# Optimization experiments

Hardware: AMD Instinct MI355X
Metric: run time of the kernel (lower is better)

The kernel has to match this reference:

```python
import jax, jax.numpy as jnp
import numpy as np

B, F, V, D_EMB = 16384, 32, 50000, 16
D_IN = F * D_EMB            # 512, concat embedding dim
N_TASK, N_SPEC, N_SH = 2, 2, 2
E = N_TASK * N_SPEC + N_SH  # 6 experts per CGC level
H1, H2 = 512, 256           # expert_params dims
T1, T2 = 128, 64            # tower dims


def setup_inputs() -> dict:
    key = jax.random.key(0)
    ks = iter(jax.random.split(key, 32))
    def w(shape, s=0.05):
        return jax.random.normal(next(ks), shape, jnp.float32) * s
    return dict(
        x_ids=jax.random.randint(next(ks), (B, F), 0, V),
        emb=w((F, V, D_EMB)),
        e1_W1=w((E, D_IN, H1)), e1_b1=jnp.zeros((E, H1), jnp.float32),
        e1_W2=w((E, H1, H2)), e1_b2=jnp.zeros((E, H2), jnp.float32),
        g1_Ws=w((N_TASK, D_IN, N_SPEC + N_SH)), g1_bs=jnp.zeros((N_TASK, N_SPEC + N_SH), jnp.float32),
        g1_Wsh=w((D_IN, E)), g1_bsh=jnp.zeros((E,), jnp.float32),
        e2_W1=w((E, H2, H1)), e2_b1=jnp.zeros((E, H1), jnp.float32),
        e2_W2=w((E, H1, H2)), e2_b2=jnp.zeros((E, H2), jnp.float32),
        g2_Ws=w((N_TASK, H2, N_SPEC + N_SH)), g2_bs=jnp.zeros((N_TASK, N_SPEC + N_SH), jnp.float32),
        tw_W1=w((N_TASK, H2, T1)), tw_b1=jnp.zeros((N_TASK, T1), jnp.float32),
        tw_W2=w((N_TASK, T1, T2)), tw_b2=jnp.zeros((N_TASK, T2), jnp.float32),
    )


def _cgc(x_list, W1, b1, W2, b2, Wg, bg, Wg_sh=None, bg_sh=None):
    # Stack expert inputs: task-t specific experts read x_list[t], shared read x_list[-1].
    X = jnp.stack([x_list[0]] * N_SPEC + [x_list[1]] * N_SPEC + [x_list[-1]] * N_SH)  # [E,B,Din]
    # Grouped two-layer expert MLP (BatchNorm is identity at eval-mode init).
    h = jax.nn.relu(jnp.einsum('ebd,edh->ebh', X, W1) + b1[:, None, :])   # [E,B,H1]
    out = jax.nn.relu(jnp.einsum('ebh,eho->ebo', h, W2) + b2[:, None, :])  # [E,B,H2]
    outs = []
    for t in range(N_TASK):
        gate = jax.nn.softmax(x_list[t] @ Wg[t] + bg[t], axis=-1)          # [B, N_SPEC+N_SH]
        sel = jnp.concatenate([out[t * N_SPEC:(t + 1) * N_SPEC], out[-N_SH:]], axis=0)
        outs.append(jnp.einsum('bk,kbo->bo', gate, sel))
    if Wg_sh is not None:  # shared gate only for levels < n_level
        gate = jax.nn.softmax(x_list[-1] @ Wg_sh + bg_sh, axis=-1)          # [B,E]
        outs.append(jnp.einsum('bk,kbo->bo', gate, out))
    return outs


def reference(x_ids, emb, e1_W1, e1_b1, e1_W2, e1_b2, g1_Ws, g1_bs, g1_Wsh, g1_bsh,
              e2_W1, e2_b1, e2_W2, e2_b2, g2_Ws, g2_bs, tw_W1, tw_b1, tw_W2, tw_b2):
    # Embedding lookup per sparse feature, then flatten (squeeze_dim=True).
    embed_x = emb[jnp.arange(F)[None, :], x_ids].reshape(B, D_IN)  # [B, 512]
    xs = [embed_x] * (N_TASK + 1)
    xs = _cgc(xs, e1_W1, e1_b1, e1_W2, e1_b2, g1_Ws, g1_bs, g1_Wsh, g1_bsh)  # level 1 -> 3 outs
    xs = _cgc(xs, e2_W1, e2_b1, e2_W2, e2_b2, g2_Ws, g2_bs)                  # level 2 -> 2 outs
    ys = []
    for t in range(N_TASK):
        h = jax.nn.relu(xs[t] @ tw_W1[t] + tw_b1[t])
        h = jax.nn.relu(h @ tw_W2[t] + tw_b2[t])
        ys.append(jax.nn.sigmoid(h))  # PredictionLayer('classification')
    return jnp.concatenate(ys, axis=1)  # [B, N_TASK*T2]
```

## Files before the change

### kernel.cpp

```cpp
#include <hip/hip_runtime.h>

typedef unsigned short u16;
typedef __attribute__((ext_vector_type(4))) unsigned short u16x4;
typedef __attribute__((ext_vector_type(8))) unsigned short u16x8;
typedef __attribute__((ext_vector_type(8))) short s16x8;
typedef __attribute__((ext_vector_type(4))) float f32x4;

#define BATCH 16384
#define NFEAT 32
#define NVOCAB 50000

__device__ __forceinline__ u16 f2bf(float f) {
    union { float f; unsigned u; } v; v.f = f;
    unsigned u = v.u;
    return (u16)((u + 0x7fffu + ((u >> 16) & 1u)) >> 16);
}
__device__ __forceinline__ float bf2f(u16 h) {
    union { unsigned u; float f; } v; v.u = ((unsigned)h) << 16;
    return v.f;
}

__device__ __forceinline__ void load_lds16(const u16* g, u16* l) {
    __builtin_amdgcn_global_load_lds(
        (const __attribute__((address_space(1))) void*)g,
        (__attribute__((address_space(3))) void*)l, 16, 0, 0);
}

struct PrepDesc { const float* src; u16* dst; int K; int N; int nz; int zbase; };
struct PrepArgs { PrepDesc d[6]; };

__global__ void prep_weights(PrepArgs args) {
    int z = blockIdx.z;
    int di = 0;
    #pragma unroll
    for (int i = 0; i < 6; i++)
        if (z >= args.d[i].zbase && z < args.d[i].zbase + args.d[i].nz) di = i;
    PrepDesc d = args.d[di];
    int zz = z - d.zbase;
    int k0 = blockIdx.x * 32, n0 = blockIdx.y * 32;
    if (k0 >= d.K || n0 >= d.N) return;
    __shared__ float tile[32][33];
    const float* src = d.src + (long)zz * d.K * d.N;
    u16* dst = d.dst + (long)zz * d.K * d.N;
    int tx = threadIdx.x & 31, ty = threadIdx.x >> 5;
    for (int r = ty; r < 32; r += 8) {
        int k = k0 + r, n = n0 + tx;
        tile[r][tx] = (k < d.K && n < d.N) ? src[(long)k * d.N + n] : 0.f;
    }
    __syncthreads();
    for (int r = ty; r < 32; r += 8) {
        int n = n0 + r, k = k0 + tx;
        if (n < d.N && k < d.K) dst[(long)n * d.K + k] = f2bf(tile[tx][r]);
    }
}

__global__ void gather_embed(const int* __restrict__ ids,
                             const float* __restrict__ emb,
                             u16* __restrict__ out) {
    int idx = blockIdx.x * 256 + threadIdx.x;
    int d4 = idx & 3;
    int f  = (idx >> 2) & 31;
    int b  = idx >> 7;
    int id = ids[b * NFEAT + f];
    const float4* p = (const float4*)(emb + ((long)f * NVOCAB + id) * 16) + d4;
    float4 v = *p;
    u16x4 o;
    o.x = f2bf(v.x); o.y = f2bf(v.y); o.z = f2bf(v.z); o.w = f2bf(v.w);
    *(u16x4*)(out + (long)b * 512 + f * 16 + d4 * 4) = o;
}

struct GemmP {
    const u16* A; const u16* Bt; const float* bias; u16* C;
    int N, K, a_zshift, c_row_stride; long a_zstride, c_zstride;
};

__device__ __forceinline__ void gemm_impl(const GemmP p) {
    __shared__ u16 sA[128 * 64];
    __shared__ u16 sB[256 * 64];
    const int z = blockIdx.z;
    const u16* Ab = p.A + (long)(z >> p.a_zshift) * p.a_zstride;
    const u16* Bb = p.Bt + (long)z * p.N * p.K;
    const int m0 = blockIdx.x * 128;
    const int n0 = blockIdx.y * 256;
    const int tid = threadIdx.x;
    const int lane = tid & 63;
    const int w = tid >> 6;
    const int wm = (w & 1) * 64;
    const int wn = (w >> 1) * 128;
    const int l16 = lane & 15;
    const int q = lane >> 4;
    const int key = l16 & 7;
    const int K = p.K;

    const int tr = tid >> 3;
    const int lc = (tid & 7) ^ (tr & 7);
    const u16* gA0 = Ab + (long)(m0 + tr) * K + lc * 8;
    const u16* gB0 = Bb + (long)(n0 + tr) * K + lc * 8;
    u16* lA0 = &sA[(tid & ~63) * 8];
    u16* lB0 = &sB[(tid & ~63) * 8];

    f32x4 acc[4][8] = {};

    for (int k0 = 0; k0 < K; k0 += 64) {
        if (k0) __syncthreads();
        #pragma unroll
        for (int i = 0; i < 4; i++)
            load_lds16(gA0 + (long)(32 * i) * K + k0, lA0 + i * 256 * 8);
        #pragma unroll
        for (int i = 0; i < 8; i++)
            load_lds16(gB0 + (long)(32 * i) * K + k0, lB0 + i * 256 * 8);
        __syncthreads();
        #pragma unroll
        for (int kk = 0; kk < 2; kk++) {
            const int pc = ((kk << 2) | q) ^ key;
            s16x8 af[4], bf[8];
            #pragma unroll
            for (int mt = 0; mt < 4; mt++)
                af[mt] = *(const s16x8*)(&sA[(wm + mt * 16 + l16) * 64 + pc * 8]);
            #pragma unroll
            for (int nt = 0; nt < 8; nt++)
                bf[nt] = *(const s16x8*)(&sB[(wn + nt * 16 + l16) * 64 + pc * 8]);
            #pragma unroll
            for (int mt = 0; mt < 4; mt++)
                #pragma unroll
                for (int nt = 0; nt < 8; nt++)
                    acc[mt][nt] = __builtin_amdgcn_mfma_f32_16x16x32_bf16(
                        bf[nt], af[mt], acc[mt][nt], 0, 0, 0);
        }
    }

    const float* bb = p.bias + (long)z * p.N;
    u16* Cp = p.C + (long)z * p.c_zstride;
    #pragma unroll
    for (int mt = 0; mt < 4; mt++) {
        int grow = m0 + wm + mt * 16 + l16;
        u16* rowp = Cp + (long)grow * p.c_row_stride;
        #pragma unroll
        for (int nt = 0; nt < 8; nt++) {
            int gc = n0 + wn + nt * 16 + q * 4;
            float4 bv = *(const float4*)(bb + gc);
            f32x4 v = acc[mt][nt];
            v.x = fmaxf(v.x + bv.x, 0.f);
            v.y = fmaxf(v.y + bv.y, 0.f);
            v.z = fmaxf(v.z + bv.z, 0.f);
            v.w = fmaxf(v.w + bv.w, 0.f);
            u16x4 o;
            o.x = f2bf(v.x); o.y = f2bf(v.y); o.z = f2bf(v.z); o.w = f2bf(v.w);
            *(u16x4*)(rowp + gc) = o;
        }
    }
}

__global__ __launch_bounds__(256, 2) void gemm_l1a(GemmP p) { gemm_impl(p); }
__global__ __launch_bounds__(256, 2) void gemm_l1b(GemmP p) { gemm_impl(p); }
__global__ __launch_bounds__(256, 2) void gemm_l2a(GemmP p) { gemm_impl(p); }
__global__ __launch_bounds__(256, 2) void gemm_l2b(GemmP p) { gemm_impl(p); }

__global__ __launch_bounds__(256, 1)
void tower_fused(const u16* __restrict__ x2, const u16* __restrict__ W1t,
                 const float* __restrict__ b1, const u16* __restrict__ W2t,
                 const float* __restrict__ b2, float* __restrict__ out) {
    const int t = blockIdx.y, m0 = blockIdx.x * 64;
    __shared__ u16 sX[64 * 256];
    __shared__ u16 sW1[128 * 256];
    __shared__ u16 sH[64 * 136];
    __shared__ u16 sW2[64 * 128];
    __shared__ float sB1[128];
    __shared__ float sB2[64];
    const int tid = threadIdx.x, lane = tid & 63, w = tid >> 6;
    const int l16 = lane & 15, q = lane >> 4;

    #pragma unroll
    for (int i = 0; i < 8; i++) {
        int c = i * 256 + tid, row = c >> 5, kc = c & 31;
        int lcc = (kc & ~7) | ((kc & 7) ^ (row & 7));
        load_lds16(x2 + ((long)t * BATCH + m0 + row) * 256 + lcc * 8,
                   &sX[(i * 256 + (tid & ~63)) * 8]);
    }
    #pragma unroll
    for (int i = 0; i < 16; i++) {
        int c = i * 256 + tid, row = c >> 5, kc = c & 31;
        int lcc = (kc & ~7) | ((kc & 7) ^ (row & 7));
        load_lds16(W1t + ((long)t * 128 + row) * 256 + lcc * 8,
                   &sW1[(i * 256 + (tid & ~63)) * 8]);
    }
    #pragma unroll
    for (int i = 0; i < 4; i++) {
        int c = i * 256 + tid, row = c >> 4, kc = c & 15;
        int lcc = (kc & ~7) | ((kc & 7) ^ (row & 7));
        load_lds16(W2t + ((long)t * 64 + row) * 128 + lcc * 8,
                   &sW2[(i * 256 + (tid & ~63)) * 8]);
    }
    if (tid < 128) sB1[tid] = b1[t * 128 + tid];
    if (tid < 64)  sB2[tid] = b2[t * 64 + tid];
    __syncthreads();

    f32x4 acc1[4][2] = {};
    #pragma unroll
    for (int kk = 0; kk < 8; kk++) {
        int pcb = kk * 4 + q;
        s16x8 af[4], bf[2];
        #pragma unroll
        for (int mt = 0; mt < 4; mt++) {
            int row = mt * 16 + l16;
            int sc = (pcb & ~7) | ((pcb & 7) ^ (row & 7));
            af[mt] = *(const s16x8*)(&sX[row * 256 + sc * 8]);
        }
        #pragma unroll
        for (int nt = 0; nt < 2; nt++) {
            int row = w * 32 + nt * 16 + l16;
            int sc = (pcb & ~7) | ((pcb & 7) ^ (row & 7));
            bf[nt] = *(const s16x8*)(&sW1[row * 256 + sc * 8]);
        }
        #pragma unroll
        for (int mt = 0; mt < 4; mt++)
            #pragma unroll
            for (int nt = 0; nt < 2; nt++)
                acc1[mt][nt] = __builtin_amdgcn_mfma_f32_16x16x32_bf16(
                    bf[nt], af[mt], acc1[mt][nt], 0, 0, 0);
    }
    #pragma unroll
    for (int mt = 0; mt < 4; mt++) {
        int row = mt * 16 + l16;
        #pragma unroll
        for (int nt = 0; nt < 2; nt++) {
            int col = w * 32 + nt * 16 + q * 4;
            f32x4 v = acc1[mt][nt];
            u16x4 o;
            o.x = f2bf(fmaxf(v.x + sB1[col + 0], 0.f));
            o.y = f2bf(fmaxf(v.y + sB1[col + 1], 0.f));
            o.z = f2bf(fmaxf(v.z + sB1[col + 2], 0.f));
            o.w = f2bf(fmaxf(v.w + sB1[col + 3], 0.f));
            *(u16x4*)(&sH[row * 136 + col]) = o;
        }
    }
    __syncthreads();

    f32x4 acc2[4] = {};
    #pragma unroll
    for (int kk = 0; kk < 4; kk++) {
        s16x8 af[4], bf;
        #pragma unroll
        for (int mt = 0; mt < 4; mt++) {
            int row = mt * 16 + l16;
            af[mt] = *(const s16x8*)(&sH[row * 136 + kk * 32 + q * 8]);
        }
        {
            int row = w * 16 + l16;
            int pc = kk * 4 + q;
            int sc = (pc & ~7) | ((pc & 7) ^ (row & 7));
            bf = *(const s16x8*)(&sW2[row * 128 + sc * 8]);
        }
        #pragma unroll
        for (int mt = 0; mt < 4; mt++)
            acc2[mt] = __builtin_amdgcn_mfma_f32_16x16x32_bf16(
                bf, af[mt], acc2[mt], 0, 0, 0);
    }
    #pragma unroll
    for (int mt = 0; mt < 4; mt++) {
        int grow = m0 + mt * 16 + l16;
        int col = w * 16 + q * 4;
        float4 bv = *(const float4*)(sB2 + col);
        f32x4 v = acc2[mt];
        float4 r;
        r.x = 1.f / (1.f + __expf(-(v.x + bv.x)));
        r.y = 1.f / (1.f + __expf(-(v.y + bv.y)));
        r.z = 1.f / (1.f + __expf(-(v.z + bv.z)));
        r.w = 1.f / (1.f + __expf(-(v.w + bv.w)));
        *(float4*)(out + (long)grow * 128 + t * 64 + col) = r;
    }
}

__global__ __launch_bounds__(256)
void gate1(const u16* __restrict__ embed, const u16* __restrict__ out1,
           const float* __restrict__ g1Ws, const float* __restrict__ g1bs,
           const float* __restrict__ gWsh, const float* __restrict__ gbsh,
           u16* __restrict__ x1) {
    const int m0 = blockIdx.x * 8;
    __shared__ float sg[8][16];
    const int tid = threadIdx.x;
    const int row = tid >> 5, l = tid & 31;
    const long rb = m0 + row;

    float a[4] = {0,0,0,0}, b[4] = {0,0,0,0}, c[6] = {0,0,0,0,0,0};
    {
        const u16* er = embed + rb * 512 + l * 16;
        u16x8 xa = *(const u16x8*)(er);
        u16x8 xb = *(const u16x8*)(er + 8);
        #pragma unroll
        for (int u = 0; u < 16; u++) {
            int k = l * 16 + u;
            float xv = bf2f(u < 8 ? xa[u] : xb[u - 8]);
            float4 wa = *(const float4*)(g1Ws + k * 4);
            float4 wb = *(const float4*)(g1Ws + 2048 + k * 4);
            a[0] += xv * wa.x; a[1] += xv * wa.y; a[2] += xv * wa.z; a[3] += xv * wa.w;
            b[0] += xv * wb.x; b[1] += xv * wb.y; b[2] += xv * wb.z; b[3] += xv * wb.w;
            float2 w0 = *(const float2*)(gWsh + k * 6);
            float2 w1 = *(const float2*)(gWsh + k * 6 + 2);
            float2 w2 = *(const float2*)(gWsh + k * 6 + 4);
            c[0] += xv * w0.x; c[1] += xv * w0.y;
            c[2] += xv * w1.x; c[3] += xv * w1.y;
            c[4] += xv * w2.x; c[5] += xv * w2.y;
        }
    }
    #pragma unroll
    for (int off = 1; off < 32; off <<= 1) {
        #pragma unroll
        for (int g = 0; g < 4; g++) { a[g] += __shfl_xor(a[g], off); b[g] += __shfl_xor(b[g], off); }
        #pragma unroll
        for (int g = 0; g < 6; g++) c[g] += __shfl_xor(c[g], off);
    }
    if (l == 0) {
        float mx, s, e[6];
        mx = -1e30f;
        for (int g = 0; g < 4; g++) { a[g] += g1bs[g]; mx = fmaxf(mx, a[g]); }
        s = 0.f; for (int g = 0; g < 4; g++) { e[g] = __expf(a[g] - mx); s += e[g]; }
        for (int g = 0; g < 4; g++) sg[row][g] = e[g] / s;
        mx = -1e30f;
        for (int g = 0; g < 4; g++) { b[g] += g1bs[4 + g]; mx = fmaxf(mx, b[g]); }
        s = 0.f; for (int g = 0; g < 4; g++) { e[g] = __expf(b[g] - mx); s += e[g]; }
        for (int g = 0; g < 4; g++) sg[row][4 + g] = e[g] / s;
        mx = -1e30f;
        for (int g = 0; g < 6; g++) { c[g] += gbsh[g]; mx = fmaxf(mx, c[g]); }
        s = 0.f; for (int g = 0; g < 6; g++) { e[g] = __expf(c[g] - mx); s += e[g]; }
        for (int g = 0; g < 6; g++) sg[row][8 + g] = e[g] / s;
    }
    __syncthreads();

    const int c8 = l * 8;
    const u16* ob = out1 + rb * 256 + c8;
    u16x8 o[6];
    #pragma unroll
    for (int k = 0; k < 6; k++) o[k] = *(const u16x8*)(ob + (long)k * BATCH * 256);
    const float* g = sg[row];
    u16x8 r0, r1, r2;
    #pragma unroll
    for (int u = 0; u < 8; u++) {
        float o0 = bf2f(o[0][u]), o1 = bf2f(o[1][u]), o2 = bf2f(o[2][u]);
        float o3 = bf2f(o[3][u]), o4 = bf2f(o[4][u]), o5 = bf2f(o[5][u]);
        r0[u] = f2bf(g[0] * o0 + g[1] * o1 + g[2] * o4 + g[3] * o5);
        r1[u] = f2bf(g[4] * o2 + g[5] * o3 + g[6] * o4 + g[7] * o5);
        r2[u] = f2bf(g[8] * o0 + g[9] * o1 + g[10] * o2 + g[11] * o3 + g[12] * o4 + g[13] * o5);
    }
    *(u16x8*)(x1 + ((long)0 * BATCH + rb) * 256 + c8) = r0;
    *(u16x8*)(x1 + ((long)1 * BATCH + rb) * 256 + c8) = r1;
    *(u16x8*)(x1 + ((long)2 * BATCH + rb) * 256 + c8) = r2;
}

__global__ __launch_bounds__(256)
void gate2(const u16* __restrict__ x1, const u16* __restrict__ out2,
           const float* __restrict__ g2Ws, const float* __restrict__ g2bs,
           u16* __restrict__ x2) {
    const int m0 = blockIdx.x * 8;
    __shared__ float sg[8][8];
    const int tid = threadIdx.x;
    const int row = tid >> 5, l = tid & 31;
    const long rb = m0 + row;

    float a[4] = {0,0,0,0}, b[4] = {0,0,0,0};
    {
        const u16* e0 = x1 + rb * 256 + l * 8;
        const u16* e1 = e0 + (long)BATCH * 256;
        u16x8 x0 = *(const u16x8*)e0;
        u16x8 x1v = *(const u16x8*)e1;
        #pragma unroll
        for (int u = 0; u < 8; u++) {
            int k = l * 8 + u;
            float4 wa = *(const float4*)(g2Ws + k * 4);
            float4 wb = *(const float4*)(g2Ws + 1024 + k * 4);
            float xv0 = bf2f(x0[u]), xv1 = bf2f(x1v[u]);
            a[0] += xv0 * wa.x; a[1] += xv0 * wa.y; a[2] += xv0 * wa.z; a[3] += xv0 * wa.w;
            b[0] += xv1 * wb.x; b[1] += xv1 * wb.y; b[2] += xv1 * wb.z; b[3] += xv1 * wb.w;
        }
    }
    #pragma unroll
    for (int off = 1; off < 32; off <<= 1) {
        #pragma unroll
        for (int g = 0; g < 4; g++) { a[g] += __shfl_xor(a[g], off); b[g] += __shfl_xor(b[g], off); }
    }
    if (l == 0) {
        float mx, s, e[4];
        mx = -1e30f;
        for (int g = 0; g < 4; g++) { a[g] += g2bs[g]; mx = fmaxf(mx, a[g]); }
        s = 0.f; for (int g = 0; g < 4; g++) { e[g] = __expf(a[g] - mx); s += e[g]; }
        for (int g = 0; g < 4; g++) sg[row][g] = e[g] / s;
        mx = -1e30f;
        for (int g = 0; g < 4; g++) { b[g] += g2bs[4 + g]; mx = fmaxf(mx, b[g]); }
        s = 0.f; for (int g = 0; g < 4; g++) { e[g] = __expf(b[g] - mx); s += e[g]; }
        for (int g = 0; g < 4; g++) sg[row][4 + g] = e[g] / s;
    }
    __syncthreads();

    const int c8 = l * 8;
    const u16* ob = out2 + rb * 256 + c8;
    u16x8 o[6];
    #pragma unroll
    for (int k = 0; k < 6; k++) o[k] = *(const u16x8*)(ob + (long)k * BATCH * 256);
    const float* g = sg[row];
    u16x8 r0, r1;
    #pragma unroll
    for (int u = 0; u < 8; u++) {
        float o0 = bf2f(o[0][u]), o1 = bf2f(o[1][u]), o2 = bf2f(o[2][u]);
        float o3 = bf2f(o[3][u]), o4 = bf2f(o[4][u]), o5 = bf2f(o[5][u]);
        r0[u] = f2bf(g[0] * o0 + g[1] * o1 + g[2] * o4 + g[3] * o5);
        r1[u] = f2bf(g[4] * o2 + g[5] * o3 + g[6] * o4 + g[7] * o5);
    }
    *(u16x8*)(x2 + ((long)0 * BATCH + rb) * 256 + c8) = r0;
    *(u16x8*)(x2 + ((long)1 * BATCH + rb) * 256 + c8) = r1;
}

extern "C" void kernel_launch(void* const* d_in, const int* in_sizes, int n_in,
                              void* d_out, int out_size, void* d_ws, size_t ws_size,
                              hipStream_t stream) {
    const int*   x_ids = (const int*)  d_in[0];
    const float* emb   = (const float*)d_in[1];
    const float* e1W1  = (const float*)d_in[2];
    const float* e1b1  = (const float*)d_in[3];
    const float* e1W2  = (const float*)d_in[4];
    const float* e1b2  = (const float*)d_in[5];
    const float* g1Ws  = (const float*)d_in[6];
    const float* g1bs  = (const float*)d_in[7];
    const float* g1Wsh = (const float*)d_in[8];
    const float* g1bsh = (const float*)d_in[9];
    const float* e2W1  = (const float*)d_in[10];
    const float* e2b1  = (const float*)d_in[11];
    const float* e2W2  = (const float*)d_in[12];
    const float* e2b2  = (const float*)d_in[13];
    const float* g2Ws  = (const float*)d_in[14];
    const float* g2bs  = (const float*)d_in[15];
    const float* twW1  = (const float*)d_in[16];
    const float* twb1  = (const float*)d_in[17];
    const float* twW2  = (const float*)d_in[18];
    const float* twb2  = (const float*)d_in[19];
    float* out = (float*)d_out;

    char* ws = (char*)d_ws;
    u16* embed   = (u16*)(ws + 0);
    u16* wt_e1W1 = (u16*)(ws + 16777216);
    u16* wt_e1W2 = (u16*)(ws + 19922944);
    u16* wt_e2W1 = (u16*)(ws + 21495808);
    u16* wt_e2W2 = (u16*)(ws + 23068672);
    u16* wt_twW1 = (u16*)(ws + 24641536);
    u16* wt_twW2 = (u16*)(ws + 24772608);
    u16* h_buf   = (u16*)(ws + 24805376);
    u16* o_buf   = (u16*)(ws + 125468672);
    u16* x1      = (u16*)(ws + 175800320);
    u16* x2      = (u16*)(ws + 200966144);

    PrepArgs pa;
    pa.d[0] = { e1W1, wt_e1W1, 512, 512, 6,  0 };
    pa.d[1] = { e1W2, wt_e1W2, 512, 256, 6,  6 };
    pa.d[2] = { e2W1, wt_e2W1, 256, 512, 6, 12 };
    pa.d[3] = { e2W2, wt_e2W2, 512, 256, 6, 18 };
    pa.d[4] = { twW1, wt_twW1, 256, 128, 2, 24 };
    pa.d[5] = { twW2, wt_twW2, 128,  64, 2, 26 };
    prep_weights<<<dim3(16, 16, 28), 256, 0, stream>>>(pa);

    gather_embed<<<dim3(BATCH * NFEAT * 4 / 256), 256, 0, stream>>>(x_ids, emb, embed);

    GemmP p1a = { embed, wt_e1W1, e1b1, h_buf, 512, 512, 0, 512, 0L, (long)BATCH * 512 };
    gemm_l1a<<<dim3(128, 2, 6), 256, 0, stream>>>(p1a);

    GemmP p1b = { h_buf, wt_e1W2, e1b2, o_buf, 256, 512, 0, 256,
                  (long)BATCH * 512, (long)BATCH * 256 };
    gemm_l1b<<<dim3(128, 1, 6), 256, 0, stream>>>(p1b);

    gate1<<<dim3(BATCH / 8), 256, 0, stream>>>(embed, o_buf, g1Ws, g1bs, g1Wsh, g1bsh, x1);

    GemmP p2a = { x1, wt_e2W1, e2b1, h_buf, 512, 256, 1, 512,
                  (long)BATCH * 256, (long)BATCH * 512 };
    gemm_l2a<<<dim3(128, 2, 6), 256, 0, stream>>>(p2a);

    GemmP p2b = { h_buf, wt_e2W2, e2b2, o_buf, 256, 512, 0, 256,
                  (long)BATCH * 512, (long)BATCH * 256 };
    gemm_l2b<<<dim3(128, 1, 6), 256, 0, stream>>>(p2b);

    gate2<<<dim3(BATCH / 8), 256, 0, stream>>>(x1, o_buf, g2Ws, g2bs, x2);

    tower_fused<<<dim3(BATCH / 64, 2), 256, 0, stream>>>(x2, wt_twW1, twb1, wt_twW2, twb2, out);
}
```

Measured before the change: 522.7 us.

## Fuse two-layer expert MLP into one kernel keeping hidden activations in LDS

Replaces the separate first- and second-layer grouped GEMM launches for each CGC level with one kernel per level. Each block loads a 64-row input tile into LDS, computes the hidden layer in 128-column chunks into LDS, and accumulates the second layer directly. This removes the round trip of the large hidden buffer through global memory and two kernel launches. In exchange, weights are read straight from global memory with no LDS staging and are reloaded by every 64-row block. The M tile is also smaller, which lowers MFMA reuse per load.

```diff
diff --git a/kernel.cpp b/kernel.cpp
--- a/kernel.cpp
+++ b/kernel.cpp
@@ -69,92 +69,130 @@
     *(u16x4*)(out + (long)b * 512 + f * 16 + d4 * 4) = o;
 }
 
-struct GemmP {
-    const u16* A; const u16* Bt; const float* bias; u16* C;
-    int N, K, a_zshift, c_row_stride; long a_zstride, c_zstride;
-};
-
-__device__ __forceinline__ void gemm_impl(const GemmP p) {
-    __shared__ u16 sA[128 * 64];
-    __shared__ u16 sB[256 * 64];
-    const int z = blockIdx.z;
-    const u16* Ab = p.A + (long)(z >> p.a_zshift) * p.a_zstride;
-    const u16* Bb = p.Bt + (long)z * p.N * p.K;
-    const int m0 = blockIdx.x * 128;
-    const int n0 = blockIdx.y * 256;
+template<int K1>
+__global__ __launch_bounds__(256, K1 == 256 ? 3 : 2)
+void fused_expert(const u16* __restrict__ A, long a_zstride, int a_zshift,
+                  const u16* __restrict__ W1t, const float* __restrict__ b1,
+                  const u16* __restrict__ W2t, const float* __restrict__ b2,
+                  u16* __restrict__ C) {
+    __shared__ u16 sA[64 * K1];
+    __shared__ u16 sH[64 * 128];
+    const int z = blockIdx.y;
+    const int m0 = blockIdx.x * 64;
+    const u16* Ab = A + (long)(z >> a_zshift) * a_zstride + (long)m0 * K1;
+    const u16* W1 = W1t + (long)z * 512 * K1;
+    const u16* W2 = W2t + (long)z * 256 * 512;
+    const float* b1z = b1 + z * 512;
+    const float* b2z = b2 + z * 256;
     const int tid = threadIdx.x;
-    const int lane = tid & 63;
-    const int w = tid >> 6;
-    const int wm = (w & 1) * 64;
-    const int wn = (w >> 1) * 128;
-    const int l16 = lane & 15;
-    const int q = lane >> 4;
-    const int key = l16 & 7;
-    const int K = p.K;
-
-    const int tr = tid >> 3;
-    const int lc = (tid & 7) ^ (tr & 7);
-    const u16* gA0 = Ab + (long)(m0 + tr) * K + lc * 8;
-    const u16* gB0 = Bb + (long)(n0 + tr) * K + lc * 8;
-    u16* lA0 = &sA[(tid & ~63) * 8];
-    u16* lB0 = &sB[(tid & ~63) * 8];
-
-    f32x4 acc[4][8] = {};
-
-    for (int k0 = 0; k0 < K; k0 += 64) {
-        if (k0) __syncthreads();
-        #pragma unroll
-        for (int i = 0; i < 4; i++)
-            load_lds16(gA0 + (long)(32 * i) * K + k0, lA0 + i * 256 * 8);
-        #pragma unroll
-        for (int i = 0; i < 8; i++)
-            load_lds16(gB0 + (long)(32 * i) * K + k0, lB0 + i * 256 * 8);
-        __syncthreads();
-        #pragma unroll
-        for (int kk = 0; kk < 2; kk++) {
-            const int pc = ((kk << 2) | q) ^ key;
-            s16x8 af[4], bf[8];
-            #pragma unroll
-            for (int mt = 0; mt < 4; mt++)
-                af[mt] = *(const s16x8*)(&sA[(wm + mt * 16 + l16) * 64 + pc * 8]);
-            #pragma unroll
-            for (int nt = 0; nt < 8; nt++)
-                bf[nt] = *(const s16x8*)(&sB[(wn + nt * 16 + l16) * 64 + pc * 8]);
+    const int lane = tid & 63, w = tid >> 6;
+    const int l16 = lane & 15, q = lane >> 4;
+
+    constexpr int CPR = K1 / 8;
+    #pragma unroll
+    for (int i = 0; i < (64 * CPR) / 256; i++) {
+        int p = i * 256 + tid;
+        int row = p / CPR;
+        int pcc = p % CPR;
+        int c = (pcc & ~7) | ((pcc & 7) ^ (row & 7));
+        load_lds16(Ab + (long)row * K1 + c * 8, &sA[(i * 256 + (tid & ~63)) * 8]);
+    }
+    __syncthreads();
+
+    f32x4 acc2[4][4] = {};
+
+    #pragma unroll 1
+    for (int nc = 0; nc < 4; nc++) {
+        f32x4 acc1[4][2] = {};
+        #pragma unroll
+        for (int kk = 0; kk < K1 / 32; kk++) {
+            s16x8 af[4], bf[2];
+            #pragma unroll
+            for (int nt = 0; nt < 2; nt++) {
+                int nrow = nc * 128 + w * 32 + nt * 16 + l16;
+                bf[nt] = *(const s16x8*)(W1 + (long)nrow * K1 + kk * 32 + q * 8);
+            }
+            #pragma unroll
+            for (int mt = 0; mt < 4; mt++) {
+                int row = mt * 16 + l16;
+                int c = kk * 4 + q;
+                int pc = (c & ~7) | ((c & 7) ^ (row & 7));
+                af[mt] = *(const s16x8*)(&sA[row * K1 + pc * 8]);
+            }
             #pragma unroll
             for (int mt = 0; mt < 4; mt++)
                 #pragma unroll
-                for (int nt = 0; nt < 8; nt++)
-                    acc[mt][nt] = __builtin_amdgcn_mfma_f32_16x16x32_bf16(
-                        bf[nt], af[mt], acc[mt][nt], 0, 0, 0);
-        }
-    }
-
-    const float* bb = p.bias + (long)z * p.N;
-    u16* Cp = p.C + (long)z * p.c_zstride;
+                for (int nt = 0; nt < 2; nt++)
+                    acc1[mt][nt] = __builtin_amdgcn_mfma_f32_16x16x32_bf16(
+                        bf[nt], af[mt], acc1[mt][nt], 0, 0, 0);
+        }
+        if (nc) __syncthreads();
+        #pragma unroll
+        for (int mt = 0; mt < 4; mt++) {
+            int row = mt * 16 + l16;
+            #pragma unroll
+            for (int nt = 0; nt < 2; nt++) {
+                int col = w * 32 + nt * 16 + q * 4;
+                float4 bv = *(const float4*)(b1z + nc * 128 + col);
+                f32x4 v = acc1[mt][nt];
+                u16x4 o;
+                o.x = f2bf(fmaxf(v.x + bv.x, 0.f));
+                o.y = f2bf(fmaxf(v.y + bv.y, 0.f));
+                o.z = f2bf(fmaxf(v.z + bv.z, 0.f));
+                o.w = f2bf(fmaxf(v.w + bv.w, 0.f));
+                int c = col >> 3;
+                int pc = (c & ~7) | ((c & 7) ^ (row & 7));
+                *(u16x4*)(&sH[row * 128 + pc * 8 + (col & 7)]) = o;
+            }
+        }
+        __syncthreads();
+        #pragma unroll
+        for (int kk = 0; kk < 4; kk++) {
+            s16x8 af[4], bf[4];
+            #pragma unroll
+            for (int nt = 0; nt < 4; nt++) {
+                int nrow = w * 64 + nt * 16 + l16;
+                bf[nt] = *(const s16x8*)(W2 + (long)nrow * 512 + nc * 128 + kk * 32 + q * 8);
+            }
+            #pragma unroll
+            for (int mt = 0; mt < 4; mt++) {
+                int row = mt * 16 + l16;
+                int c = kk * 4 + q;
+                int pc = (c & ~7) | ((c & 7) ^ (row & 7));
+                af[mt] = *(const s16x8*)(&sH[row * 128 + pc * 8]);
+            }
+            #pragma unroll
+            for (int mt = 0; mt < 4; mt++)
+                #pragma unroll
+                for (int nt = 0; nt < 4; nt++)
+                    acc2[mt][nt] = __builtin_amdgcn_mfma_f32_16x16x32_bf16(
+                        bf[nt], af[mt], acc2[mt][nt], 0, 0, 0);
+        }
+    }
+
+    u16* Cp = C + (long)z * BATCH * 256;
     #pragma unroll
     for (int mt = 0; mt < 4; mt++) {
-        int grow = m0 + wm + mt * 16 + l16;
-        u16* rowp = Cp + (long)grow * p.c_row_stride;
-        #pragma unroll
-        for (int nt = 0; nt < 8; nt++) {
-            int gc = n0 + wn + nt * 16 + q * 4;
-            float4 bv = *(const float4*)(bb + gc);
-            f32x4 v = acc[mt][nt];
-            v.x = fmaxf(v.x + bv.x, 0.f);
-            v.y = fmaxf(v.y + bv.y, 0.f);
-            v.z = fmaxf(v.z + bv.z, 0.f);
-            v.w = fmaxf(v.w + bv.w, 0.f);
+        int grow = m0 + mt * 16 + l16;
+        u16* rowp = Cp + (long)grow * 256;
+        #pragma unroll
+        for (int nt = 0; nt < 4; nt++) {
+            int gc = w * 64 + nt * 16 + q * 4;
+            float4 bv = *(const float4*)(b2z + gc);
+            f32x4 v = acc2[mt][nt];
             u16x4 o;
-            o.x = f2bf(v.x); o.y = f2bf(v.y); o.z = f2bf(v.z); o.w = f2bf(v.w);
+            o.x = f2bf(fmaxf(v.x + bv.x, 0.f));
+            o.y = f2bf(fmaxf(v.y + bv.y, 0.f));
+            o.z = f2bf(fmaxf(v.z + bv.z, 0.f));
+            o.w = f2bf(fmaxf(v.w + bv.w, 0.f));
             *(u16x4*)(rowp + gc) = o;
         }
     }
 }
 
-__global__ __launch_bounds__(256, 2) void gemm_l1a(GemmP p) { gemm_impl(p); }
-__global__ __launch_bounds__(256, 2) void gemm_l1b(GemmP p) { gemm_impl(p); }
-__global__ __launch_bounds__(256, 2) void gemm_l2a(GemmP p) { gemm_impl(p); }
-__global__ __launch_bounds__(256, 2) void gemm_l2b(GemmP p) { gemm_impl(p); }
+__global__ __launch_bounds__(256, 2)
+void fused_l1(const u16* A, const u16* W1t, const float* b1,
+              const u16* W2t, const float* b2, u16* C);
 
 __global__ __launch_bounds__(256, 1)
 void tower_fused(const u16* __restrict__ x2, const u16* __restrict__ W1t,
@@ -442,7 +480,6 @@
     u16* wt_e2W2 = (u16*)(ws + 23068672);
     u16* wt_twW1 = (u16*)(ws + 24641536);
     u16* wt_twW2 = (u16*)(ws + 24772608);
-    u16* h_buf   = (u16*)(ws + 24805376);
     u16* o_buf   = (u16*)(ws + 125468672);
     u16* x1      = (u16*)(ws + 175800320);
     u16* x2      = (u16*)(ws + 200966144);
@@ -458,22 +495,13 @@
 
     gather_embed<<<dim3(BATCH * NFEAT * 4 / 256), 256, 0, stream>>>(x_ids, emb, embed);
 
-    GemmP p1a = { embed, wt_e1W1, e1b1, h_buf, 512, 512, 0, 512, 0L, (long)BATCH * 512 };
-    gemm_l1a<<<dim3(128, 2, 6), 256, 0, stream>>>(p1a);
-
-    GemmP p1b = { h_buf, wt_e1W2, e1b2, o_buf, 256, 512, 0, 256,
-                  (long)BATCH * 512, (long)BATCH * 256 };
-    gemm_l1b<<<dim3(128, 1, 6), 256, 0, stream>>>(p1b);
+    fused_expert<512><<<dim3(BATCH / 64, 6), 256, 0, stream>>>(
+        embed, 0L, 3, wt_e1W1, e1b1, wt_e1W2, e1b2, o_buf);
 
     gate1<<<dim3(BATCH / 8), 256, 0, stream>>>(embed, o_buf, g1Ws, g1bs, g1Wsh, g1bsh, x1);
 
-    GemmP p2a = { x1, wt_e2W1, e2b1, h_buf, 512, 256, 1, 512,
-                  (long)BATCH * 256, (long)BATCH * 512 };
-    gemm_l2a<<<dim3(128, 2, 6), 256, 0, stream>>>(p2a);
-
-    GemmP p2b = { h_buf, wt_e2W2, e2b2, o_buf, 256, 512, 0, 256,
-                  (long)BATCH * 512, (long)BATCH * 256 };
-    gemm_l2b<<<dim3(128, 1, 6), 256, 0, stream>>>(p2b);
+    fused_expert<256><<<dim3(BATCH / 64, 6), 256, 0, stream>>>(
+        x1, (long)BATCH * 256, 1, wt_e2W1, e2b1, wt_e2W2, e2b2, o_buf);
 
     gate2<<<dim3(BATCH / 8), 256, 0, stream>>>(x1, o_buf, g2Ws, g2bs, x2);
 
```

After: 559.1 us. +7.0%, slower.
